# Performance work log

Hardware: AMD Instinct MI355X
Metric: run time of the kernel (lower is better)

The kernel has to match this reference:

```python
import jax, jax.numpy as jnp
import numpy as np

N = 100000       # nodes
E = 1600000      # edges (avg degree 16)
F_IN = 128
F_HID = 64
F_OUT = 40
K = 10
ALPHA = 0.1


def setup_inputs() -> dict:
    key = jax.random.key(0)
    k1, k2, k3, k4, k5, k6 = jax.random.split(key, 6)
    x = jax.random.normal(k1, (N, F_IN), dtype=jnp.float32)
    edge_index = jax.random.randint(k2, (2, E), 0, N, dtype=jnp.int32)
    # Linear params (Kaiming-uniform-ish scale)
    W1 = jax.random.normal(k3, (F_IN, F_HID), dtype=jnp.float32) / np.sqrt(F_IN)
    b1 = jax.random.normal(k4, (F_HID,), dtype=jnp.float32) * 0.01
    W2 = jax.random.normal(k5, (F_HID, F_OUT), dtype=jnp.float32) / np.sqrt(F_HID)
    b2 = jax.random.normal(k6, (F_OUT,), dtype=jnp.float32) * 0.01
    return {"x": x, "edge_index": edge_index, "W1": W1, "b1": b1, "W2": W2, "b2": b2}


def _gcn_norm(edge_index, dtype):
    # add self loops, symmetric normalization D^{-1/2} (A+I) D^{-1/2}
    loops = jnp.arange(N, dtype=edge_index.dtype)
    src = jnp.concatenate([edge_index[0], loops])
    dst = jnp.concatenate([edge_index[1], loops])
    deg = jax.ops.segment_sum(jnp.ones_like(src, dtype=dtype), dst, num_segments=N)
    dinv = jnp.where(deg > 0, jax.lax.rsqrt(deg), 0.0).astype(dtype)
    norm = dinv[src] * dinv[dst]  # [E + N]
    return src, dst, norm


def _appnp(x, src, dst, norm):
    h = x  # teleport target
    def step(xc, _):
        agg = jax.ops.segment_sum(xc[src] * norm[:, None], dst, num_segments=N)
        return (1.0 - ALPHA) * agg + ALPHA * h, None
    out, _ = jax.lax.scan(step, x, None, length=K)
    return out


def reference(x, edge_index, W1, b1, W2, b2):
    src, dst, norm = _gcn_norm(edge_index, x.dtype)
    # layer 1: Linear -> relu -> (dropout p=0) -> APPNP
    h = jax.nn.relu(x @ W1 + b1)
    h = _appnp(h, src, dst, norm)
    # layer 2: Linear -> relu -> APPNP
    h = jax.nn.relu(h @ W2 + b2)
    h = _appnp(h, src, dst, norm)
    return jax.nn.log_softmax(h, axis=1)
```

## Files before the change

kernel.cpp:

```cpp
#include <hip/hip_runtime.h>
#include <hip/hip_fp16.h>
#include <hip/hip_fp8.h>

namespace {
constexpr int NN = 100000;
constexpr int NE = 1600000;
constexpr int FIN = 128, FHID = 64, FOUT = 40;
constexpr float ALPHA = 0.1f;
constexpr int SLOTS = 64;
constexpr int SB = 40;
constexpr int ECHUNK = 200000;

typedef int v4i __attribute__((ext_vector_type(4)));
typedef unsigned int v2u __attribute__((ext_vector_type(2)));
typedef unsigned int v4u __attribute__((ext_vector_type(4)));
typedef float v2f __attribute__((ext_vector_type(2)));
typedef float v4f __attribute__((ext_vector_type(4)));
typedef _Float16 half8 __attribute__((ext_vector_type(8)));

#if __has_builtin(__builtin_amdgcn_cvt_pk_f32_fp8) && __has_builtin(__builtin_amdgcn_cvt_pk_fp8_f32)
#define HW_FP8 1
#else
#define HW_FP8 0
#endif

__device__ __forceinline__ ushort f2h(float v) {
  union { __half h; ushort u; } cv;
  cv.h = __float2half_rn(v);
  return cv.u;
}

__device__ __forceinline__ void acc8_fp8(v2u w, float* a) {
#if HW_FP8
  v2f p0 = __builtin_amdgcn_cvt_pk_f32_fp8((int)w.x, false);
  v2f p1 = __builtin_amdgcn_cvt_pk_f32_fp8((int)w.x, true);
  v2f p2 = __builtin_amdgcn_cvt_pk_f32_fp8((int)w.y, false);
  v2f p3 = __builtin_amdgcn_cvt_pk_f32_fp8((int)w.y, true);
  a[0] += p0.x; a[1] += p0.y; a[2] += p1.x; a[3] += p1.y;
  a[4] += p2.x; a[5] += p2.y; a[6] += p3.x; a[7] += p3.y;
#else
  union { v2u w; unsigned char b[8]; } cv;
  cv.w = w;
#pragma unroll
  for (int k = 0; k < 8; k++) {
    __hip_fp8_e4m3 h;
    h.__x = cv.b[k];
    a[k] += (float)h;
  }
#endif
}

__device__ __forceinline__ v2u enc8_fp8(const float* o) {
#if HW_FP8
  int d0 = __builtin_amdgcn_cvt_pk_fp8_f32(o[0], o[1], 0, false);
  d0 = __builtin_amdgcn_cvt_pk_fp8_f32(o[2], o[3], d0, true);
  int d1 = __builtin_amdgcn_cvt_pk_fp8_f32(o[4], o[5], 0, false);
  d1 = __builtin_amdgcn_cvt_pk_fp8_f32(o[6], o[7], d1, true);
  v2u r;
  r.x = (unsigned int)d0;
  r.y = (unsigned int)d1;
  return r;
#else
  union { v2u w; unsigned char b[8]; } cv;
#pragma unroll
  for (int k = 0; k < 8; k++) {
    __hip_fp8_e4m3 h(o[k]);
    cv.b[k] = h.__x;
  }
  return cv.w;
#endif
}

__device__ __forceinline__ unsigned int enc4_fp8(float a, float b, float c, float d) {
#if HW_FP8
  int d0 = __builtin_amdgcn_cvt_pk_fp8_f32(a, b, 0, false);
  d0 = __builtin_amdgcn_cvt_pk_fp8_f32(c, d, d0, true);
  return (unsigned int)d0;
#else
  union { unsigned char b4[4]; unsigned int u; } cv;
  __hip_fp8_e4m3 h0(a), h1(b), h2(c), h3(d);
  cv.b4[0] = h0.__x; cv.b4[1] = h1.__x; cv.b4[2] = h2.__x; cv.b4[3] = h3.__x;
  return cv.u;
#endif
}

__global__ void k_zero(int* cnt) {
  int i = blockIdx.x * 256 + threadIdx.x;
  if (i < NN) cnt[i] = 0;
}

__global__ void k_fill_ell(const int* __restrict__ src, const int* __restrict__ dst,
                           int* __restrict__ cnt, int* __restrict__ ell, int ebase) {
  int e = ebase + blockIdx.x * 256 + threadIdx.x;
  if (e >= ebase + ECHUNK || e >= NE) return;
  int s = src[e], d = dst[e];
  int p = atomicAdd(&cnt[d], 1);
  if (p < SLOTS) ell[(d << 6) + p] = s;
}

__global__ void k_dinv(const int* __restrict__ cnt, float2* __restrict__ dd) {
  int i = blockIdx.x * 256 + threadIdx.x;
  if (i < NN) {
    float di = rsqrtf((float)(cnt[i] + 1));
    dd[i] = make_float2(di, 0.9f * di * di);
  }
}

__global__ __launch_bounds__(256, 3) void k_mlp(const float* __restrict__ x,
                                                const float* __restrict__ W1,
                                                const float* __restrict__ b1,
                                                const float* __restrict__ W2,
                                                const float2* __restrict__ dd,
                                                float* __restrict__ h2x,
                                                ushort* __restrict__ u0,
                                                unsigned char* __restrict__ uq) {
  __shared__ _Float16 w1t[64 * 136];
  __shared__ _Float16 w2t[48 * 72];
  __shared__ unsigned int ht[4 * 16 * 36];

  int tid = threadIdx.x;
  for (int i = tid; i < 2048; i += 256) {
    float4 v = ((const float4*)W1)[i];
    int k = i >> 4;
    int c0 = (i & 15) * 4;
    w1t[(c0 + 0) * 136 + k] = (_Float16)v.x;
    w1t[(c0 + 1) * 136 + k] = (_Float16)v.y;
    w1t[(c0 + 2) * 136 + k] = (_Float16)v.z;
    w1t[(c0 + 3) * 136 + k] = (_Float16)v.w;
  }
  for (int i = tid; i < 2560; i += 256) {
    int k = i / 40, c = i - k * 40;
    w2t[c * 72 + k] = (_Float16)W2[i];
  }
  for (int i = tid; i < 576; i += 256) w2t[2880 + i] = (_Float16)0.f;
  __syncthreads();

  int wid = tid >> 6, lane = tid & 63;
  int g = lane >> 4, n = lane & 15;
  int node = blockIdx.x * 64 + wid * 16 + n;
  int nodeL = node < NN ? node : NN - 1;
  const float* xr = x + (size_t)nodeL * FIN;

  v4f acc1[4] = {};
#pragma unroll
  for (int kk = 0; kk < 4; kk++) {
    const float4* xp = (const float4*)(xr + kk * 32 + g * 8);
    float4 xa = xp[0], xb = xp[1];
    half8 bx;
    bx[0] = (_Float16)xa.x; bx[1] = (_Float16)xa.y;
    bx[2] = (_Float16)xa.z; bx[3] = (_Float16)xa.w;
    bx[4] = (_Float16)xb.x; bx[5] = (_Float16)xb.y;
    bx[6] = (_Float16)xb.z; bx[7] = (_Float16)xb.w;
#pragma unroll
    for (int mt = 0; mt < 4; mt++) {
      half8 af = *(const half8*)(w1t + (mt * 16 + n) * 136 + kk * 32 + g * 8);
      acc1[mt] = __builtin_amdgcn_mfma_f32_16x16x32_f16(af, bx, acc1[mt], 0, 0, 0);
    }
  }

  unsigned int* hw = ht + wid * 576 + n * 36;
#pragma unroll
  for (int mt = 0; mt < 4; mt++) {
    float4 bb = *(const float4*)(b1 + mt * 16 + g * 4);
    union { _Float16 h[4]; uint2 u; } pk;
    pk.h[0] = (_Float16)fmaxf(acc1[mt][0] + bb.x, 0.f);
    pk.h[1] = (_Float16)fmaxf(acc1[mt][1] + bb.y, 0.f);
    pk.h[2] = (_Float16)fmaxf(acc1[mt][2] + bb.z, 0.f);
    pk.h[3] = (_Float16)fmaxf(acc1[mt][3] + bb.w, 0.f);
    *(uint2*)(hw + mt * 8 + g * 2) = pk.u;
  }

  v4f acc2[3] = {};
#pragma unroll
  for (int kk = 0; kk < 2; kk++) {
    half8 bh = *(const half8*)((const _Float16*)(hw + kk * 16 + g * 4));
#pragma unroll
    for (int mt2 = 0; mt2 < 3; mt2++) {
      half8 af = *(const half8*)(w2t + (mt2 * 16 + n) * 72 + kk * 32 + g * 8);
      acc2[mt2] = __builtin_amdgcn_mfma_f32_16x16x32_f16(af, bh, acc2[mt2], 0, 0, 0);
    }
  }

  if (node < NN) {
    float di = dd[node].x;
#pragma unroll
    for (int mt2 = 0; mt2 < 3; mt2++) {
      int c0 = mt2 * 16 + g * 4;
      if (c0 < FOUT) {
        float y0 = acc2[mt2][0], y1 = acc2[mt2][1];
        float y2 = acc2[mt2][2], y3 = acc2[mt2][3];
        *(float4*)(h2x + (size_t)node * FOUT + c0) = make_float4(y0, y1, y2, y3);
        float u0v = di * y0, u1v = di * y1, u2v = di * y2, u3v = di * y3;
        union { ushort s[4]; uint2 q; } hq;
        hq.s[0] = f2h(u0v); hq.s[1] = f2h(u1v);
        hq.s[2] = f2h(u2v); hq.s[3] = f2h(u3v);
        *(uint2*)(u0 + (size_t)node * FOUT + c0) = hq.q;
        *(unsigned int*)(uq + (size_t)node * SB + c0) = enc4_fp8(u0v, u1v, u2v, u3v);
      }
    }
  }
}

__device__ __forceinline__ void gather_ell(const int* __restrict__ ell,
                                           const unsigned char* __restrict__ u,
                                           int node, int ch, int deg, float* a) {
#pragma unroll
  for (int k = 0; k < 8; k++) a[k] = 0.f;
  const unsigned char* ub = u + ch * 8;
  const v4i* ip = (const v4i*)ell + ((size_t)node << 4);
  v2u ws = *(const v2u*)(ub + (size_t)node * SB);
  v4i q0 = ip[0];
  v4i q1 = ip[1];
  acc8_fp8(ws, a);
  int j = 0;
  for (; j + 8 <= deg; j += 8) {
    int g = (j >> 2) + 2;
    v4i n0 = ip[g > 15 ? 15 : g];
    v4i n1 = ip[g + 1 > 15 ? 15 : g + 1];
    v2u w0 = *(const v2u*)(ub + (size_t)q0.x * SB);
    v2u w1 = *(const v2u*)(ub + (size_t)q0.y * SB);
    v2u w2 = *(const v2u*)(ub + (size_t)q0.z * SB);
    v2u w3 = *(const v2u*)(ub + (size_t)q0.w * SB);
    v2u w4 = *(const v2u*)(ub + (size_t)q1.x * SB);
    v2u w5 = *(const v2u*)(ub + (size_t)q1.y * SB);
    v2u w6 = *(const v2u*)(ub + (size_t)q1.z * SB);
    v2u w7 = *(const v2u*)(ub + (size_t)q1.w * SB);
    acc8_fp8(w0, a);
    acc8_fp8(w1, a);
    acc8_fp8(w2, a);
    acc8_fp8(w3, a);
    acc8_fp8(w4, a);
    acc8_fp8(w5, a);
    acc8_fp8(w6, a);
    acc8_fp8(w7, a);
    q0 = n0;
    q1 = n1;
  }
  if (j + 4 <= deg) {
    v2u w0 = *(const v2u*)(ub + (size_t)q0.x * SB);
    v2u w1 = *(const v2u*)(ub + (size_t)q0.y * SB);
    v2u w2 = *(const v2u*)(ub + (size_t)q0.z * SB);
    v2u w3 = *(const v2u*)(ub + (size_t)q0.w * SB);
    acc8_fp8(w0, a);
    acc8_fp8(w1, a);
    acc8_fp8(w2, a);
    acc8_fp8(w3, a);
    q0 = q1;
    j += 4;
  }
  if (j < deg) {
    int rr = deg - j;
    acc8_fp8(*(const v2u*)(ub + (size_t)q0.x * SB), a);
    if (rr > 1) acc8_fp8(*(const v2u*)(ub + (size_t)q0.y * SB), a);
    if (rr > 2) acc8_fp8(*(const v2u*)(ub + (size_t)q0.z * SB), a);
  }
}

#define APPNP_HDR(cntp)                            \
  int tid = threadIdx.x;                           \
  int nd = tid / 5, ch = tid - nd * 5;             \
  int node = blockIdx.x * 64 + nd;                 \
  if (node >= NN) return;                          \
  int deg = (cntp)[node];                          \
  deg = deg > SLOTS ? SLOTS : deg;

__device__ __forceinline__ void store_h8(ushort* p, const float* v) {
  union { v4u u; __half h[8]; } cv;
#pragma unroll
  for (int k = 0; k < 8; k++) cv.h[k] = __float2half_rn(v[k]);
  *(v4u*)p = cv.u;
}

__global__ __launch_bounds__(320, 6) void k_mid(const int* __restrict__ cnt,
                                                const int* __restrict__ ell,
                                                const float2* __restrict__ dd,
                                                const ushort* __restrict__ u0,
                                                const unsigned char* __restrict__ u,
                                                unsigned char* __restrict__ un) {
  APPNP_HDR(cnt)
  union { v4u q; __half h[8]; } t0;
  t0.q = *(const v4u*)(u0 + (size_t)node * FOUT + ch * 8);
  float c9 = dd[node].y;
  float a[8];
  gather_ell(ell, u, node, ch, deg, a);
  float o[8];
#pragma unroll
  for (int k = 0; k < 8; k++) o[k] = c9 * a[k] + ALPHA * __half2float(t0.h[k]);
  v2u st = enc8_fp8(o);
  *(v2u*)(un + (size_t)node * SB + ch * 8) = st;
}

__global__ __launch_bounds__(320, 6) void k_final1(const int* __restrict__ cnt,
                                                   const int* __restrict__ ell,
                                                   const float2* __restrict__ dd,
                                                   const float* __restrict__ b2,
                                                   const float* __restrict__ h2x,
                                                   const unsigned char* __restrict__ u,
                                                   ushort* __restrict__ gh,
                                                   ushort* __restrict__ u0n,
                                                   unsigned char* __restrict__ uqn) {
  APPNP_HDR(cnt)
  float di = dd[node].x;
  v4f h0 = __builtin_nontemporal_load((const v4f*)(h2x + (size_t)node * FOUT + ch * 8));
  v4f h1 = __builtin_nontemporal_load((const v4f*)(h2x + (size_t)node * FOUT + ch * 8 + 4));
  const float* bb = b2 + ch * 8;
  float a[8];
  gather_ell(ell, u, node, ch, deg, a);
  float t9 = 0.9f * di;
  float hx[8] = {h0.x, h0.y, h0.z, h0.w, h1.x, h1.y, h1.z, h1.w};
  float g[8], ug[8];
#pragma unroll
  for (int k = 0; k < 8; k++) {
    float z = t9 * a[k] + ALPHA * hx[k] + bb[k];
    g[k] = fmaxf(z, 0.f);
    ug[k] = di * g[k];
  }
  store_h8(gh + (size_t)node * FOUT + ch * 8, g);
  store_h8(u0n + (size_t)node * FOUT + ch * 8, ug);
  v2u st = enc8_fp8(ug);
  *(v2u*)(uqn + (size_t)node * SB + ch * 8) = st;
}

__global__ __launch_bounds__(320, 6) void k_final2(const int* __restrict__ cnt,
                                                   const int* __restrict__ ell,
                                                   const float2* __restrict__ dd,
                                                   const ushort* __restrict__ gh,
                                                   const unsigned char* __restrict__ u,
                                                   ushort* __restrict__ zh) {
  APPNP_HDR(cnt)
  union { v4u q; __half h[8]; } hv;
  hv.q = *(const v4u*)(gh + (size_t)node * FOUT + ch * 8);
  float t9 = 0.9f * dd[node].x;
  float a[8];
  gather_ell(ell, u, node, ch, deg, a);
  float o[8];
#pragma unroll
  for (int k = 0; k < 8; k++) o[k] = t9 * a[k] + ALPHA * __half2float(hv.h[k]);
  store_h8(zh + (size_t)node * FOUT + ch * 8, o);
}

__global__ void k_logsoftmax(const ushort* __restrict__ in, float* __restrict__ out) {
  int i = blockIdx.x * 256 + threadIdx.x;
  if (i >= NN) return;
  union { v4u q; __half h[8]; } v[5];
  const v4u* r = (const v4u*)(in + (size_t)i * FOUT);
  float f[40];
  float m = -1e30f;
#pragma unroll
  for (int j = 0; j < 5; j++) {
    v[j].q = r[j];
#pragma unroll
    for (int k = 0; k < 8; k++) {
      f[j * 8 + k] = __half2float(v[j].h[k]);
      m = fmaxf(m, f[j * 8 + k]);
    }
  }
  float sum = 0.f;
#pragma unroll
  for (int j = 0; j < 40; j++) sum += expf(f[j] - m);
  float lse = m + logf(sum);
  float4* o = (float4*)(out + (size_t)i * FOUT);
#pragma unroll
  for (int j = 0; j < 10; j++) {
    float4 w = {f[j * 4] - lse, f[j * 4 + 1] - lse, f[j * 4 + 2] - lse, f[j * 4 + 3] - lse};
    o[j] = w;
  }
}

}

extern "C" void kernel_launch(void* const* d_in, const int* in_sizes, int n_in,
                              void* d_out, int out_size, void* d_ws, size_t ws_size,
                              hipStream_t stream) {
  const float* x = (const float*)d_in[0];
  const int* ei = (const int*)d_in[1];
  const int* src = ei;
  const int* dst = ei + NE;
  const float* W1 = (const float*)d_in[2];
  const float* b1 = (const float*)d_in[3];
  const float* W2 = (const float*)d_in[4];
  const float* b2 = (const float*)d_in[5];
  float* out = (float*)d_out;

  char* ws = (char*)d_ws;
  size_t off = 0;
  auto alloc = [&](size_t bytes) -> void* {
    void* p = ws + off;
    off += (bytes + 255) & ~(size_t)255;
    return p;
  };
  int* cnt          = (int*)alloc((size_t)NN * 4);
  float2* dd        = (float2*)alloc((size_t)NN * 8);
  int* ell          = (int*)alloc((size_t)NN * SLOTS * 4);
  float* h2x        = (float*)alloc((size_t)NN * FOUT * 4);
  ushort* u0h       = (ushort*)alloc((size_t)NN * FOUT * 2);
  ushort* gh        = (ushort*)alloc((size_t)NN * FOUT * 2);
  ushort* zh        = (ushort*)alloc((size_t)NN * FOUT * 2);
  unsigned char* q0 = (unsigned char*)alloc((size_t)NN * SB);
  unsigned char* qA = (unsigned char*)alloc((size_t)NN * SB);
  unsigned char* qB = (unsigned char*)alloc((size_t)NN * SB);

  k_zero<<<(NN + 255) / 256, 256, 0, stream>>>(cnt);
  for (int c = 0; c < NE / ECHUNK; c++)
    k_fill_ell<<<(ECHUNK + 255) / 256, 256, 0, stream>>>(src, dst, cnt, ell, c * ECHUNK);
  k_dinv<<<(NN + 255) / 256, 256, 0, stream>>>(cnt, dd);

  k_mlp<<<(NN + 63) / 64, 256, 0, stream>>>(x, W1, b1, W2, dd, h2x, u0h, q0);

  int agrid = (NN + 63) / 64;
  const unsigned char* cu = q0;
  for (int it = 0; it < 9; it++) {
    unsigned char* nx = (it & 1) ? qB : qA;
    k_mid<<<agrid, 320, 0, stream>>>(cnt, ell, dd, u0h, cu, nx);
    cu = nx;
  }
  k_final1<<<agrid, 320, 0, stream>>>(cnt, ell, dd, b2, h2x, cu, gh, u0h, q0);

  cu = q0;
  for (int it = 0; it < 9; it++) {
    unsigned char* nx = (it & 1) ? qB : qA;
    k_mid<<<agrid, 320, 0, stream>>>(cnt, ell, dd, u0h, cu, nx);
    cu = nx;
  }
  k_final2<<<agrid, 320, 0, stream>>>(cnt, ell, dd, gh, cu, zh);

  k_logsoftmax<<<(NN + 255) / 256, 256, 0, stream>>>(zh, out);
}
```

Before: 653.6 us.

## Sort nodes by degree via counting sort to balance APPNP gather work

Builds a permutation of nodes grouped by in-degree (histogram, prefix, scatter) and makes the APPNP kernels process nodes in that order, so the nodes in a wavefront have similar gather loop lengths and less divergence. It also merges the chunked edge-fill launches into one launch. The cost is three extra small kernels, including a single-thread prefix, plus an indirect perm load. Per-node reads and writes are no longer contiguous across neighbouring threads, which hurts coalescing.

```diff
diff --git a/kernel.cpp b/kernel.cpp
--- a/kernel.cpp
+++ b/kernel.cpp
@@ -9,7 +9,6 @@
 constexpr float ALPHA = 0.1f;
 constexpr int SLOTS = 64;
 constexpr int SB = 40;
-constexpr int ECHUNK = 200000;
 
 typedef int v4i __attribute__((ext_vector_type(4)));
 typedef unsigned int v2u __attribute__((ext_vector_type(2)));
@@ -84,15 +83,16 @@
 #endif
 }
 
-__global__ void k_zero(int* cnt) {
+__global__ void k_zero(int* cnt, int* bins) {
   int i = blockIdx.x * 256 + threadIdx.x;
   if (i < NN) cnt[i] = 0;
+  if (i <= SLOTS) bins[i] = 0;
 }
 
 __global__ void k_fill_ell(const int* __restrict__ src, const int* __restrict__ dst,
-                           int* __restrict__ cnt, int* __restrict__ ell, int ebase) {
-  int e = ebase + blockIdx.x * 256 + threadIdx.x;
-  if (e >= ebase + ECHUNK || e >= NE) return;
+                           int* __restrict__ cnt, int* __restrict__ ell) {
+  int e = blockIdx.x * 256 + threadIdx.x;
+  if (e >= NE) return;
   int s = src[e], d = dst[e];
   int p = atomicAdd(&cnt[d], 1);
   if (p < SLOTS) ell[(d << 6) + p] = s;
@@ -103,6 +103,33 @@
   if (i < NN) {
     float di = rsqrtf((float)(cnt[i] + 1));
     dd[i] = make_float2(di, 0.9f * di * di);
+  }
+}
+
+__global__ void k_hist(const int* __restrict__ cnt, int* __restrict__ bins) {
+  int i = blockIdx.x * 256 + threadIdx.x;
+  if (i < NN) {
+    int d = cnt[i];
+    d = d > SLOTS ? SLOTS : d;
+    atomicAdd(&bins[d], 1);
+  }
+}
+
+__global__ void k_prefix(const int* __restrict__ bins, int* __restrict__ boff) {
+  if (threadIdx.x == 0 && blockIdx.x == 0) {
+    int s = 0;
+    for (int d = 0; d <= SLOTS; d++) { boff[d] = s; s += bins[d]; }
+  }
+}
+
+__global__ void k_scatter(const int* __restrict__ cnt, int* __restrict__ boff,
+                          int* __restrict__ perm) {
+  int i = blockIdx.x * 256 + threadIdx.x;
+  if (i < NN) {
+    int d = cnt[i];
+    d = d > SLOTS ? SLOTS : d;
+    int p = atomicAdd(&boff[d], 1);
+    perm[p] = i;
   }
 }
 
@@ -256,11 +283,12 @@
   }
 }
 
-#define APPNP_HDR(cntp)                            \
+#define APPNP_HDR(cntp, permp)                     \
   int tid = threadIdx.x;                           \
   int nd = tid / 5, ch = tid - nd * 5;             \
-  int node = blockIdx.x * 64 + nd;                 \
-  if (node >= NN) return;                          \
+  int slot = blockIdx.x * 64 + nd;                 \
+  if (slot >= NN) return;                          \
+  int node = (permp)[slot];                        \
   int deg = (cntp)[node];                          \
   deg = deg > SLOTS ? SLOTS : deg;
 
@@ -272,12 +300,13 @@
 }
 
 __global__ __launch_bounds__(320, 6) void k_mid(const int* __restrict__ cnt,
+                                                const int* __restrict__ perm,
                                                 const int* __restrict__ ell,
                                                 const float2* __restrict__ dd,
                                                 const ushort* __restrict__ u0,
                                                 const unsigned char* __restrict__ u,
                                                 unsigned char* __restrict__ un) {
-  APPNP_HDR(cnt)
+  APPNP_HDR(cnt, perm)
   union { v4u q; __half h[8]; } t0;
   t0.q = *(const v4u*)(u0 + (size_t)node * FOUT + ch * 8);
   float c9 = dd[node].y;
@@ -291,6 +320,7 @@
 }
 
 __global__ __launch_bounds__(320, 6) void k_final1(const int* __restrict__ cnt,
+                                                   const int* __restrict__ perm,
                                                    const int* __restrict__ ell,
                                                    const float2* __restrict__ dd,
                                                    const float* __restrict__ b2,
@@ -299,7 +329,7 @@
                                                    ushort* __restrict__ gh,
                                                    ushort* __restrict__ u0n,
                                                    unsigned char* __restrict__ uqn) {
-  APPNP_HDR(cnt)
+  APPNP_HDR(cnt, perm)
   float di = dd[node].x;
   v4f h0 = __builtin_nontemporal_load((const v4f*)(h2x + (size_t)node * FOUT + ch * 8));
   v4f h1 = __builtin_nontemporal_load((const v4f*)(h2x + (size_t)node * FOUT + ch * 8 + 4));
@@ -322,12 +352,13 @@
 }
 
 __global__ __launch_bounds__(320, 6) void k_final2(const int* __restrict__ cnt,
+                                                   const int* __restrict__ perm,
                                                    const int* __restrict__ ell,
                                                    const float2* __restrict__ dd,
                                                    const ushort* __restrict__ gh,
                                                    const unsigned char* __restrict__ u,
                                                    ushort* __restrict__ zh) {
-  APPNP_HDR(cnt)
+  APPNP_HDR(cnt, perm)
   union { v4u q; __half h[8]; } hv;
   hv.q = *(const v4u*)(gh + (size_t)node * FOUT + ch * 8);
   float t9 = 0.9f * dd[node].x;
@@ -399,11 +430,17 @@
   unsigned char* q0 = (unsigned char*)alloc((size_t)NN * SB);
   unsigned char* qA = (unsigned char*)alloc((size_t)NN * SB);
   unsigned char* qB = (unsigned char*)alloc((size_t)NN * SB);
-
-  k_zero<<<(NN + 255) / 256, 256, 0, stream>>>(cnt);
-  for (int c = 0; c < NE / ECHUNK; c++)
-    k_fill_ell<<<(ECHUNK + 255) / 256, 256, 0, stream>>>(src, dst, cnt, ell, c * ECHUNK);
+  int* perm         = (int*)alloc((size_t)NN * 4);
+  int* bins         = (int*)alloc(256);
+  int* boff         = (int*)alloc(256);
+
+  k_zero<<<(NN + 255) / 256, 256, 0, stream>>>(cnt, bins);
+  k_fill_ell<<<(NE + 255) / 256, 256, 0, stream>>>(src, dst, cnt, ell);
   k_dinv<<<(NN + 255) / 256, 256, 0, stream>>>(cnt, dd);
+
+  k_hist<<<(NN + 255) / 256, 256, 0, stream>>>(cnt, bins);
+  k_prefix<<<1, 64, 0, stream>>>(bins, boff);
+  k_scatter<<<(NN + 255) / 256, 256, 0, stream>>>(cnt, boff, perm);
 
   k_mlp<<<(NN + 63) / 64, 256, 0, stream>>>(x, W1, b1, W2, dd, h2x, u0h, q0);
 
@@ -411,18 +448,18 @@
   const unsigned char* cu = q0;
   for (int it = 0; it < 9; it++) {
     unsigned char* nx = (it & 1) ? qB : qA;
-    k_mid<<<agrid, 320, 0, stream>>>(cnt, ell, dd, u0h, cu, nx);
+    k_mid<<<agrid, 320, 0, stream>>>(cnt, perm, ell, dd, u0h, cu, nx);
     cu = nx;
   }
-  k_final1<<<agrid, 320, 0, stream>>>(cnt, ell, dd, b2, h2x, cu, gh, u0h, q0);
+  k_final1<<<agrid, 320, 0, stream>>>(cnt, perm, ell, dd, b2, h2x, cu, gh, u0h, q0);
 
   cu = q0;
   for (int it = 0; it < 9; it++) {
     unsigned char* nx = (it & 1) ? qB : qA;
-    k_mid<<<agrid, 320, 0, stream>>>(cnt, ell, dd, u0h, cu, nx);
+    k_mid<<<agrid, 320, 0, stream>>>(cnt, perm, ell, dd, u0h, cu, nx);
     cu = nx;
   }
-  k_final2<<<agrid, 320, 0, stream>>>(cnt, ell, dd, gh, cu, zh);
+  k_final2<<<agrid, 320, 0, stream>>>(cnt, perm, ell, dd, gh, cu, zh);
 
   k_logsoftmax<<<(NN + 255) / 256, 256, 0, stream>>>(zh, out);
 }
```

Measured after the change: 1.328 ms. 2.03x slower.

## Switch ELL neighbor table from row-major to slot-major layout

Applied to the files above, without the earlier changes.

Stores the ELL adjacency as slot-major (slot * N + node) instead of node-major 64-slot rows, and rewrites the gather to read eight slot entries per step with scalar loads. The goal is coalesced index loads across adjacent nodes in a wavefront, replacing 16-byte vector loads that stride 256 bytes between nodes. In exchange, the five threads sharing a node issue redundant scalar loads, and each step loads more individual index words.

```diff
diff --git a/kernel.cpp b/kernel.cpp
--- a/kernel.cpp
+++ b/kernel.cpp
@@ -95,7 +95,7 @@
   if (e >= ebase + ECHUNK || e >= NE) return;
   int s = src[e], d = dst[e];
   int p = atomicAdd(&cnt[d], 1);
-  if (p < SLOTS) ell[(d << 6) + p] = s;
+  if (p < SLOTS) ell[(size_t)p * NN + d] = s;
 }
 
 __global__ void k_dinv(const int* __restrict__ cnt, float2* __restrict__ dd) {
@@ -201,58 +201,37 @@
   }
 }
 
-__device__ __forceinline__ void gather_ell(const int* __restrict__ ell,
-                                           const unsigned char* __restrict__ u,
-                                           int node, int ch, int deg, float* a) {
+__device__ __forceinline__ void gather_pm(const int* __restrict__ ell,
+                                          const unsigned char* __restrict__ u,
+                                          int node, int ch, int deg, float* a) {
 #pragma unroll
   for (int k = 0; k < 8; k++) a[k] = 0.f;
   const unsigned char* ub = u + ch * 8;
-  const v4i* ip = (const v4i*)ell + ((size_t)node << 4);
   v2u ws = *(const v2u*)(ub + (size_t)node * SB);
-  v4i q0 = ip[0];
-  v4i q1 = ip[1];
+  int q[8], qn[8];
+#pragma unroll
+  for (int k = 0; k < 8; k++) q[k] = ell[(size_t)k * NN + node];
   acc8_fp8(ws, a);
   int j = 0;
   for (; j + 8 <= deg; j += 8) {
-    int g = (j >> 2) + 2;
-    v4i n0 = ip[g > 15 ? 15 : g];
-    v4i n1 = ip[g + 1 > 15 ? 15 : g + 1];
-    v2u w0 = *(const v2u*)(ub + (size_t)q0.x * SB);
-    v2u w1 = *(const v2u*)(ub + (size_t)q0.y * SB);
-    v2u w2 = *(const v2u*)(ub + (size_t)q0.z * SB);
-    v2u w3 = *(const v2u*)(ub + (size_t)q0.w * SB);
-    v2u w4 = *(const v2u*)(ub + (size_t)q1.x * SB);
-    v2u w5 = *(const v2u*)(ub + (size_t)q1.y * SB);
-    v2u w6 = *(const v2u*)(ub + (size_t)q1.z * SB);
-    v2u w7 = *(const v2u*)(ub + (size_t)q1.w * SB);
-    acc8_fp8(w0, a);
-    acc8_fp8(w1, a);
-    acc8_fp8(w2, a);
-    acc8_fp8(w3, a);
-    acc8_fp8(w4, a);
-    acc8_fp8(w5, a);
-    acc8_fp8(w6, a);
-    acc8_fp8(w7, a);
-    q0 = n0;
-    q1 = n1;
-  }
-  if (j + 4 <= deg) {
-    v2u w0 = *(const v2u*)(ub + (size_t)q0.x * SB);
-    v2u w1 = *(const v2u*)(ub + (size_t)q0.y * SB);
-    v2u w2 = *(const v2u*)(ub + (size_t)q0.z * SB);
-    v2u w3 = *(const v2u*)(ub + (size_t)q0.w * SB);
-    acc8_fp8(w0, a);
-    acc8_fp8(w1, a);
-    acc8_fp8(w2, a);
-    acc8_fp8(w3, a);
-    q0 = q1;
-    j += 4;
-  }
-  if (j < deg) {
-    int rr = deg - j;
-    acc8_fp8(*(const v2u*)(ub + (size_t)q0.x * SB), a);
-    if (rr > 1) acc8_fp8(*(const v2u*)(ub + (size_t)q0.y * SB), a);
-    if (rr > 2) acc8_fp8(*(const v2u*)(ub + (size_t)q0.z * SB), a);
+#pragma unroll
+    for (int k = 0; k < 8; k++) {
+      int pl = j + 8 + k;
+      pl = pl > SLOTS - 1 ? SLOTS - 1 : pl;
+      qn[k] = ell[(size_t)pl * NN + node];
+    }
+    v2u w[8];
+#pragma unroll
+    for (int k = 0; k < 8; k++) w[k] = *(const v2u*)(ub + (size_t)q[k] * SB);
+#pragma unroll
+    for (int k = 0; k < 8; k++) acc8_fp8(w[k], a);
+#pragma unroll
+    for (int k = 0; k < 8; k++) q[k] = qn[k];
+  }
+  int rr = deg - j;
+#pragma unroll
+  for (int k = 0; k < 7; k++) {
+    if (k < rr) acc8_fp8(*(const v2u*)(ub + (size_t)q[k] * SB), a);
   }
 }
 
@@ -282,7 +261,7 @@
   t0.q = *(const v4u*)(u0 + (size_t)node * FOUT + ch * 8);
   float c9 = dd[node].y;
   float a[8];
-  gather_ell(ell, u, node, ch, deg, a);
+  gather_pm(ell, u, node, ch, deg, a);
   float o[8];
 #pragma unroll
   for (int k = 0; k < 8; k++) o[k] = c9 * a[k] + ALPHA * __half2float(t0.h[k]);
@@ -305,7 +284,7 @@
   v4f h1 = __builtin_nontemporal_load((const v4f*)(h2x + (size_t)node * FOUT + ch * 8 + 4));
   const float* bb = b2 + ch * 8;
   float a[8];
-  gather_ell(ell, u, node, ch, deg, a);
+  gather_pm(ell, u, node, ch, deg, a);
   float t9 = 0.9f * di;
   float hx[8] = {h0.x, h0.y, h0.z, h0.w, h1.x, h1.y, h1.z, h1.w};
   float g[8], ug[8];
@@ -332,7 +311,7 @@
   hv.q = *(const v4u*)(gh + (size_t)node * FOUT + ch * 8);
   float t9 = 0.9f * dd[node].x;
   float a[8];
-  gather_ell(ell, u, node, ch, deg, a);
+  gather_pm(ell, u, node, ch, deg, a);
   float o[8];
 #pragma unroll
   for (int k = 0; k < 8; k++) o[k] = t9 * a[k] + ALPHA * __half2float(hv.h[k]);
```

New measurement: 638.3 us. -2.3%, faster.
